# Kernel optimization log

Hardware: AMD Instinct MI355X
Metric: run time of the kernel (lower is better)

## Reference

```python
import jax, jax.numpy as jnp
import numpy as np

NEG_SLOPE = 0.2  # PyG GATConv default leaky_relu slope
N_NODES, IN_DIM, HID, HEADS, OUT = 50000, 128, 64, 4, 128
N_EDGES = 800000


def gat_conv(x, src, dst, num_nodes, W, a_src, a_dst, bias, concat):
    """One PyG-style GATConv (add_self_loops already applied to src/dst)."""
    H, C = a_src.shape
    xp = (x @ W).reshape(num_nodes, H, C)            # (N,H,C)
    s = jnp.einsum('nhc,hc->nh', xp, a_src)          # per-node src score
    d = jnp.einsum('nhc,hc->nh', xp, a_dst)          # per-node dst score
    e = s[src] + d[dst]                              # (E,H)
    e = jnp.where(e > 0, e, NEG_SLOPE * e)           # leaky_relu
    # segment softmax over edges grouped by destination node
    m = jax.ops.segment_max(e, dst, num_segments=num_nodes)
    p = jnp.exp(e - m[dst])
    z = jax.ops.segment_sum(p, dst, num_segments=num_nodes)
    alpha = p / (z[dst] + 1e-16)                     # (E,H)
    # scatter-aggregate messages
    out = jax.ops.segment_sum(xp[src] * alpha[:, :, None], dst, num_segments=num_nodes)
    out = out.reshape(num_nodes, H * C) if concat else out.mean(axis=1)
    return out + bias


def setup_inputs() -> dict:
    key = jax.random.key(0)
    ks = jax.random.split(key, 16)
    HC = HEADS * HID
    inp = {
        'x': jax.random.normal(ks[0], (N_NODES, IN_DIM), dtype=jnp.float32),
        'edge_index': jax.random.randint(ks[1], (2, N_EDGES), 0, N_NODES, dtype=jnp.int32),
        'W0': jax.random.normal(ks[2], (IN_DIM, HC), dtype=jnp.float32) * 0.08,
        'a_src0': jax.random.normal(ks[3], (HEADS, HID), dtype=jnp.float32) * 0.1,
        'a_dst0': jax.random.normal(ks[4], (HEADS, HID), dtype=jnp.float32) * 0.1,
        'b0': jnp.zeros((HC,), dtype=jnp.float32),
        'W1': jax.random.normal(ks[5], (HC, HC), dtype=jnp.float32) * 0.06,
        'a_src1': jax.random.normal(ks[6], (HEADS, HID), dtype=jnp.float32) * 0.1,
        'a_dst1': jax.random.normal(ks[7], (HEADS, HID), dtype=jnp.float32) * 0.1,
        'b1': jnp.zeros((HC,), dtype=jnp.float32),
        'W2': jax.random.normal(ks[8], (HC, OUT), dtype=jnp.float32) * 0.06,
        'a_src2': jax.random.normal(ks[9], (1, OUT), dtype=jnp.float32) * 0.1,
        'a_dst2': jax.random.normal(ks[10], (1, OUT), dtype=jnp.float32) * 0.1,
        'b2': jnp.zeros((OUT,), dtype=jnp.float32),
    }
    return inp


def reference(x, edge_index, W0, a_src0, a_dst0, b0, W1, a_src1, a_dst1, b1, W2, a_src2, a_dst2, b2):
    N = x.shape[0]
    loops = jnp.arange(N, dtype=edge_index.dtype)  # add_self_loops=True
    src = jnp.concatenate([edge_index[0], loops])
    dst = jnp.concatenate([edge_index[1], loops])
    h = gat_conv(x, src, dst, N, W0, a_src0, a_dst0, b0, True)
    h = jax.nn.elu(h)
    h = gat_conv(h, src, dst, N, W1, a_src1, a_dst1, b1, True)
    h = jax.nn.elu(h)
    h = gat_conv(h, src, dst, N, W2, a_src2, a_dst2, b2, False)
    return h
```

## Files before the change

### kernel.cpp

```cpp
#include <hip/hip_runtime.h>
#include <hip/hip_bf16.h>
#include <hip/hip_fp16.h>
#include <math.h>

#define N_NODES 50000
#define N_EDGES 800000
#define ET      (N_EDGES + N_NODES)
#define IN_DIM  128
#define HEADS   4
#define HID     64
#define HC      256
#define OUTD    128

typedef _Float16 half8 __attribute__((ext_vector_type(8)));
typedef float f32x4 __attribute__((ext_vector_type(4)));


__global__ void scan1_k(const int* __restrict__ counts, int* __restrict__ offs,
                        int* __restrict__ bsums) {
    __shared__ int sm[512];
    int tid = threadIdx.x;
    int i = blockIdx.x * 512 + tid;
    int v = (i < N_NODES) ? counts[i] : 0;
    sm[tid] = v;
    __syncthreads();
    #pragma unroll
    for (int o = 1; o < 512; o <<= 1) {
        int add = (tid >= o) ? sm[tid - o] : 0;
        __syncthreads();
        sm[tid] += add;
        __syncthreads();
    }
    if (i < N_NODES) offs[i] = sm[tid] - v;
    if (tid == 511) bsums[blockIdx.x] = sm[511];
}

__global__ void scan3_k(int* __restrict__ offs, const int* __restrict__ bsums) {
    __shared__ int base_sm;
    int tid = threadIdx.x;
    if (tid < 64) {
        int p = 0;
        for (int j = tid; j < (int)blockIdx.x; j += 64) p += bsums[j];
        #pragma unroll
        for (int o = 1; o < 64; o <<= 1) p += __shfl_xor(p, o, 64);
        if (tid == 0) base_sm = p;
    }
    __syncthreads();
    int i = blockIdx.x * 512 + tid;
    if (i < N_NODES) offs[i] += base_sm;
    if (i == 0) offs[N_NODES] = ET;
}

__global__ void fill_k(const int* __restrict__ ei, const int* __restrict__ offs,
                       int* __restrict__ counts, int* __restrict__ csr) {
    int i = blockIdx.x * blockDim.x + threadIdx.x;
    if (i >= ET) return;
    int sv, dv;
    if (i < N_EDGES) { sv = ei[i]; dv = ei[N_EDGES + i]; }
    else             { sv = dv = i - N_EDGES; }
    int pos = offs[dv] + atomicSub(&counts[dv], 1) - 1;
    csr[pos] = sv;
}


#define J_HIST  ET
#define J_CVT   (N_NODES * IN_DIM / 4)
#define J_W     131072
#define SETUP_TOTAL (J_HIST + J_CVT + J_W + 2 * N_NODES)

__global__ void setup_k(const int* __restrict__ ei, int* __restrict__ counts,
                        const float* __restrict__ x, __half* __restrict__ xh,
                        const float* __restrict__ W0, __half* __restrict__ Wt0,
                        const float* __restrict__ W1, __half* __restrict__ Wt1,
                        const float* __restrict__ W2, __half* __restrict__ Wt2,
                        float* __restrict__ S2, float* __restrict__ D2) {
    int g = blockIdx.x * 256 + threadIdx.x;
    if (g < J_HIST) {
        int dv = (g < N_EDGES) ? ei[N_EDGES + g] : (g - N_EDGES);
        atomicAdd(&counts[dv], 1);
        return;
    }
    g -= J_HIST;
    if (g < J_CVT) {
        float4 v = *(const float4*)(x + (size_t)g * 4);
        union { __half2 h2[2]; float2 f2; } u;
        u.h2[0] = __floats2half2_rn(v.x, v.y);
        u.h2[1] = __floats2half2_rn(v.z, v.w);
        *(float2*)(xh + (size_t)g * 4) = u.f2;
        return;
    }
    g -= J_CVT;
    if (g < J_W) {
        if (g < 32768) {
            int n = g / IN_DIM, k = g - n * IN_DIM;
            Wt0[g] = __float2half(W0[(size_t)k * HC + n]);
        } else if (g < 98304) {
            int i = g - 32768;
            int n = i / HC, k = i - n * HC;
            Wt1[i] = __float2half(W1[(size_t)k * HC + n]);
        } else {
            int i = g - 98304;
            int n = i / HC, k = i - n * HC;
            Wt2[i] = __float2half(W2[(size_t)k * OUTD + n]);
        }
        return;
    }
    g -= J_W;
    if (g < N_NODES) { S2[g] = 0.f; return; }
    g -= N_NODES;
    if (g < N_NODES) D2[g] = 0.f;
}


__device__ __forceinline__ void async_copy16(void* lds_base, const void* gaddr) {
    __builtin_amdgcn_global_load_lds(
        (const __attribute__((address_space(1))) unsigned int*)gaddr,
        (__attribute__((address_space(3))) unsigned int*)lds_base,
        16, 0, 0);
}

#define CPAD 132

template<int H, int CD, bool ATOMIC>
__global__ __launch_bounds__(256) void gemm_mfma_k(const __half* __restrict__ A,
                                                   const __half* __restrict__ Wt,
                                                   __half* __restrict__ C,
                                                   const float* __restrict__ asrc,
                                                   const float* __restrict__ adst,
                                                   float* __restrict__ S,
                                                   float* __restrict__ D,
                                                   int M, int K, int N) {
    __shared__ __attribute__((aligned(16))) __half smem[128 * CPAD];
    __half* Ah = smem;
    __half* Bh = smem + 128 * 64;
    const int t = threadIdx.x;
    const int w = t >> 6;
    const int lane = t & 63;
    const int wm = w >> 1, wn = w & 1;
    const int cc = lane & 15;
    const int quad = lane >> 4;
    const int row0 = blockIdx.x * 128;
    const int col0 = blockIdx.y * 128;

    f32x4 acc[4][4];
    #pragma unroll
    for (int i = 0; i < 4; ++i)
        #pragma unroll
        for (int j = 0; j < 4; ++j) acc[i][j] = (f32x4){0.f, 0.f, 0.f, 0.f};

    const int srow = lane >> 3;
    const int skq  = (lane & 7) * 8;

    for (int k0 = 0; k0 < K; k0 += 64) {
        __syncthreads();
        #pragma unroll
        for (int hh = 0; hh < 4; ++hh) {
            int ra = row0 + w * 32 + hh * 8 + srow;
            if (ra > M - 1) ra = M - 1;
            async_copy16(&Ah[(w * 32 + hh * 8) * 64],
                         A + (size_t)ra * K + k0 + skq);
            int rb = col0 + w * 32 + hh * 8 + srow;
            async_copy16(&Bh[(w * 32 + hh * 8) * 64],
                         Wt + (size_t)rb * K + k0 + skq);
        }
        __syncthreads();
        #pragma unroll
        for (int c = 0; c < 2; ++c) {
            half8 a[4], b[4];
            #pragma unroll
            for (int i = 0; i < 4; ++i)
                a[i] = *(const half8*)&Ah[(wm * 64 + i * 16 + cc) * 64 + c * 32 + quad * 8];
            #pragma unroll
            for (int j = 0; j < 4; ++j)
                b[j] = *(const half8*)&Bh[(wn * 64 + j * 16 + cc) * 64 + c * 32 + quad * 8];
            #pragma unroll
            for (int i = 0; i < 4; ++i)
                #pragma unroll
                for (int j = 0; j < 4; ++j)
                    acc[i][j] = __builtin_amdgcn_mfma_f32_16x16x32_f16(b[j], a[i], acc[i][j], 0, 0, 0);
        }
    }

    const int hh_ = ATOMIC ? 0 : (blockIdx.y * 2 + wn);
    float4 asj[4], adj[4];
    #pragma unroll
    for (int j = 0; j < 4; ++j) {
        int cb = (ATOMIC ? wn * 64 : 0) + j * 16 + quad * 4;
        asj[j] = *(const float4*)&asrc[hh_ * CD + cb];
        adj[j] = *(const float4*)&adst[hh_ * CD + cb];
    }
    #pragma unroll
    for (int i = 0; i < 4; ++i) {
        float sv = 0.f, dv = 0.f;
        #pragma unroll
        for (int j = 0; j < 4; ++j) {
            sv = fmaf(acc[i][j][0], asj[j].x, sv); dv = fmaf(acc[i][j][0], adj[j].x, dv);
            sv = fmaf(acc[i][j][1], asj[j].y, sv); dv = fmaf(acc[i][j][1], adj[j].y, dv);
            sv = fmaf(acc[i][j][2], asj[j].z, sv); dv = fmaf(acc[i][j][2], adj[j].z, dv);
            sv = fmaf(acc[i][j][3], asj[j].w, sv); dv = fmaf(acc[i][j][3], adj[j].w, dv);
        }
        sv += __shfl_xor(sv, 16, 64); dv += __shfl_xor(dv, 16, 64);
        sv += __shfl_xor(sv, 32, 64); dv += __shfl_xor(dv, 32, 64);
        int r = row0 + wm * 64 + i * 16 + cc;
        if (quad == 0 && r < M) {
            if constexpr (ATOMIC) {
                atomicAdd(&S[r], sv);
                atomicAdd(&D[r], dv);
            } else {
                S[(size_t)r * H + hh_] = sv;
                D[(size_t)r * H + hh_] = dv;
            }
        }
    }

    __syncthreads();
    #pragma unroll
    for (int i = 0; i < 4; ++i) {
        int tr = wm * 64 + i * 16 + cc;
        #pragma unroll
        for (int j = 0; j < 4; ++j) {
            int tc = wn * 64 + j * 16 + quad * 4;
            union { __half2 h2[2]; uint2 u2; } pk;
            pk.h2[0] = __floats2half2_rn(acc[i][j][0], acc[i][j][1]);
            pk.h2[1] = __floats2half2_rn(acc[i][j][2], acc[i][j][3]);
            *(uint2*)&smem[tr * CPAD + tc] = pk.u2;
        }
    }
    __syncthreads();
    #pragma unroll
    for (int rr = 0; rr < 8; ++rr) {
        int r = rr * 16 + (t >> 4);
        int ccol = (t & 15) * 8;
        uint4 v = *(const uint4*)&smem[r * CPAD + ccol];
        int gr = row0 + r;
        if (gr < M)
            *(uint4*)&C[(size_t)gr * N + col0 + ccol] = v;
    }
}


template<int H, int C, bool ELU_OUT, typename OT>
__global__ __launch_bounds__(256) void aggr_k(const __half* __restrict__ xp,
                                              const float* __restrict__ s,
                                              const float* __restrict__ d,
                                              const int* __restrict__ offs,
                                              const int* __restrict__ csr,
                                              const float* __restrict__ bias,
                                              OT* __restrict__ out) {
    constexpr int HCl = H * C;
    constexpr int EPL = HCl / 64;
    constexpr int U = 8;
    int wid = blockIdx.x * 4 + (threadIdx.x >> 6);
    int lane = threadIdx.x & 63;
    if (wid >= N_NODES) return;
    int h = (lane * EPL) / C;
    float dh = d[(size_t)wid * H + h];
    float z = 0.f;
    float acc[EPL];
    #pragma unroll
    for (int k = 0; k < EPL; ++k) acc[k] = 0.f;

    auto loadrow = [&](int src, float* v) {
        const __half* xr = xp + (size_t)src * HCl + lane * EPL;
        if constexpr (EPL == 4) {
            union { float2 f2; __half2 h2[2]; } u;
            u.f2 = *(const float2*)xr;
            float2 a = __half22float2(u.h2[0]);
            float2 b = __half22float2(u.h2[1]);
            v[0] = a.x; v[1] = a.y; v[2] = b.x; v[3] = b.y;
        } else {
            union { float f; __half2 h2; } u;
            u.f = *(const float*)xr;
            float2 a = __half22float2(u.h2);
            v[0] = a.x; v[1] = a.y;
        }
    };

    int e0 = offs[wid], e1 = offs[wid + 1];
    int j = e0;
    for (; j + U <= e1; j += U) {
        int srcs[U];
        #pragma unroll
        for (int u = 0; u < U; ++u) srcs[u] = csr[j + u];
        float ev[U];
        #pragma unroll
        for (int u = 0; u < U; ++u) ev[u] = s[(size_t)srcs[u] * H + h];
        float v[U][EPL];
        #pragma unroll
        for (int u = 0; u < U; ++u) loadrow(srcs[u], v[u]);
        #pragma unroll
        for (int u = 0; u < U; ++u) {
            float e = ev[u] + dh;
            e = (e > 0.f) ? e : 0.2f * e;
            float p = __expf(e);
            z += p;
            #pragma unroll
            for (int k = 0; k < EPL; ++k) acc[k] += p * v[u][k];
        }
    }
    for (; j < e1; ++j) {
        int sv = csr[j];
        float e = s[(size_t)sv * H + h] + dh;
        e = (e > 0.f) ? e : 0.2f * e;
        float p = __expf(e);
        float v[EPL];
        loadrow(sv, v);
        z += p;
        #pragma unroll
        for (int k = 0; k < EPL; ++k) acc[k] += p * v[k];
    }

    float inv = 1.f / (z + 1e-16f);
    float o[EPL];
    #pragma unroll
    for (int k = 0; k < EPL; ++k) {
        o[k] = acc[k] * inv + bias[lane * EPL + k];
        if constexpr (ELU_OUT) o[k] = (o[k] > 0.f) ? o[k] : (__expf(o[k]) - 1.f);
    }
    if constexpr (sizeof(OT) == 2 && EPL == 4) {
        union { __half2 h2[2]; float2 f2; } u;
        u.h2[0] = __floats2half2_rn(o[0], o[1]);
        u.h2[1] = __floats2half2_rn(o[2], o[3]);
        *(float2*)((__half*)out + (size_t)wid * HCl + lane * EPL) = u.f2;
    } else {
        #pragma unroll
        for (int k = 0; k < EPL; ++k)
            out[(size_t)wid * HCl + lane * EPL + k] = (OT)o[k];
    }
}


extern "C" void kernel_launch(void* const* d_in, const int* in_sizes, int n_in,
                              void* d_out, int out_size, void* d_ws, size_t ws_size,
                              hipStream_t stream) {
    const float* x      = (const float*)d_in[0];
    const int*   ei     = (const int*)  d_in[1];
    const float* W0     = (const float*)d_in[2];
    const float* as0    = (const float*)d_in[3];
    const float* ad0    = (const float*)d_in[4];
    const float* b0     = (const float*)d_in[5];
    const float* W1     = (const float*)d_in[6];
    const float* as1    = (const float*)d_in[7];
    const float* ad1    = (const float*)d_in[8];
    const float* b1     = (const float*)d_in[9];
    const float* W2     = (const float*)d_in[10];
    const float* as2    = (const float*)d_in[11];
    const float* ad2    = (const float*)d_in[12];
    const float* b2     = (const float*)d_in[13];
    float* out = (float*)d_out;

    char* p = (char*)d_ws;
    auto take = [&](size_t bytes) {
        char* r = p;
        p += (bytes + 255) & ~(size_t)255;
        return r;
    };
    __half* XPh   = (__half*)take((size_t)N_NODES * HC * 2);
    __half* Hbuf  = (__half*)take((size_t)N_NODES * HC * 2);
    __half* xh    = (__half*)take((size_t)N_NODES * IN_DIM * 2);
    __half* Wt0   = (__half*)take((size_t)IN_DIM * HC * 2);
    __half* Wt1   = (__half*)take((size_t)HC * HC * 2);
    __half* Wt2   = (__half*)take((size_t)HC * OUTD * 2);
    float*  S     = (float*) take((size_t)N_NODES * HEADS * 4);
    float*  D     = (float*) take((size_t)N_NODES * HEADS * 4);
    float*  S2    = (float*) take((size_t)N_NODES * 4);
    float*  D2    = (float*) take((size_t)N_NODES * 4);
    int*    counts= (int*)   take((size_t)N_NODES * 4);
    int*    offs  = (int*)   take((size_t)(N_NODES + 1) * 4);
    int*    bsums = (int*)   take(512 * 4);
    int*    csr   = (int*)   take((size_t)ET * 4);

    const int NB_SCAN = (N_NODES + 511) / 512;
    const int ET_BLOCKS = (ET + 255) / 256;
    const int NODE_BLOCKS = (N_NODES + 3) / 4;
    const int MB = (N_NODES + 127) / 128;
    dim3 g0(MB, HC / 128);
    dim3 g2(MB, OUTD / 128);

    hipMemsetAsync(counts, 0, (size_t)N_NODES * 4, stream);
    setup_k<<<(SETUP_TOTAL + 255) / 256, 256, 0, stream>>>(
        ei, counts, x, xh, W0, Wt0, W1, Wt1, W2, Wt2, S2, D2);

    scan1_k<<<NB_SCAN, 512, 0, stream>>>(counts, offs, bsums);
    scan3_k<<<NB_SCAN, 512, 0, stream>>>(offs, bsums);
    fill_k<<<ET_BLOCKS, 256, 0, stream>>>(ei, offs, counts, csr);

    gemm_mfma_k<HEADS, HID, false><<<g0, 256, 0, stream>>>(xh, Wt0, XPh, as0, ad0, S, D, N_NODES, IN_DIM, HC);
    aggr_k<HEADS, HID, true, __half><<<NODE_BLOCKS, 256, 0, stream>>>(XPh, S, D, offs, csr, b0, Hbuf);

    gemm_mfma_k<HEADS, HID, false><<<g0, 256, 0, stream>>>(Hbuf, Wt1, XPh, as1, ad1, S, D, N_NODES, HC, HC);
    aggr_k<HEADS, HID, true, __half><<<NODE_BLOCKS, 256, 0, stream>>>(XPh, S, D, offs, csr, b1, Hbuf);

    gemm_mfma_k<1, OUTD, true><<<g2, 256, 0, stream>>>(Hbuf, Wt2, XPh, as2, ad2, S2, D2, N_NODES, HC, OUTD);
    aggr_k<1, OUTD, false, float><<<NODE_BLOCKS, 256, 0, stream>>>(XPh, S2, D2, offs, csr, b2, out);
}
```

Baseline: 413.4 us.

## Split wavefront into two half-waves processing alternate edges with wider loads

The aggregation kernel now splits each 64-lane wavefront into two 32-lane halves. Each half handles alternate edges of the destination node, and each lane loads 8 or 4 halves per row (16- or 8-byte vector loads) instead of 4 or 2. Partial sums are combined with a cross-half shuffle, and the remainder loop is replaced by predicated masking that sets the score of out-of-range edges to a large negative value. The aim is more memory parallelism per wave and wider gathers, at the cost of padded wasted work on short edge lists and an extra reduction.

```diff
diff --git a/kernel.cpp b/kernel.cpp
--- a/kernel.cpp
+++ b/kernel.cpp
@@ -248,84 +248,96 @@
                                               const float* __restrict__ bias,
                                               OT* __restrict__ out) {
     constexpr int HCl = H * C;
-    constexpr int EPL = HCl / 64;
+    constexpr int FPL = HCl / 32;
     constexpr int U = 8;
-    int wid = blockIdx.x * 4 + (threadIdx.x >> 6);
-    int lane = threadIdx.x & 63;
+    const int tid = threadIdx.x;
+    const int lane = tid & 63;
+    const int l = lane & 31;
+    const int par = lane >> 5;
+    int wid = blockIdx.x * 4 + (tid >> 6);
     if (wid >= N_NODES) return;
-    int h = (lane * EPL) / C;
-    float dh = d[(size_t)wid * H + h];
+    const int h = (l * FPL) / C;
+    const int loff = l * FPL;
+
+    float dh = d[wid * H + h];
     float z = 0.f;
-    float acc[EPL];
-    #pragma unroll
-    for (int k = 0; k < EPL; ++k) acc[k] = 0.f;
-
-    auto loadrow = [&](int src, float* v) {
-        const __half* xr = xp + (size_t)src * HCl + lane * EPL;
-        if constexpr (EPL == 4) {
-            union { float2 f2; __half2 h2[2]; } u;
-            u.f2 = *(const float2*)xr;
-            float2 a = __half22float2(u.h2[0]);
-            float2 b = __half22float2(u.h2[1]);
-            v[0] = a.x; v[1] = a.y; v[2] = b.x; v[3] = b.y;
-        } else {
-            union { float f; __half2 h2; } u;
-            u.f = *(const float*)xr;
-            float2 a = __half22float2(u.h2);
-            v[0] = a.x; v[1] = a.y;
-        }
-    };
-
-    int e0 = offs[wid], e1 = offs[wid + 1];
-    int j = e0;
-    for (; j + U <= e1; j += U) {
-        int srcs[U];
-        #pragma unroll
-        for (int u = 0; u < U; ++u) srcs[u] = csr[j + u];
-        float ev[U];
-        #pragma unroll
-        for (int u = 0; u < U; ++u) ev[u] = s[(size_t)srcs[u] * H + h];
-        float v[U][EPL];
-        #pragma unroll
-        for (int u = 0; u < U; ++u) loadrow(srcs[u], v[u]);
-        #pragma unroll
-        for (int u = 0; u < U; ++u) {
-            float e = ev[u] + dh;
-            e = (e > 0.f) ? e : 0.2f * e;
-            float p = __expf(e);
-            z += p;
-            #pragma unroll
-            for (int k = 0; k < EPL; ++k) acc[k] += p * v[u][k];
-        }
-    }
-    for (; j < e1; ++j) {
-        int sv = csr[j];
-        float e = s[(size_t)sv * H + h] + dh;
-        e = (e > 0.f) ? e : 0.2f * e;
-        float p = __expf(e);
-        float v[EPL];
-        loadrow(sv, v);
-        z += p;
-        #pragma unroll
-        for (int k = 0; k < EPL; ++k) acc[k] += p * v[k];
-    }
+    float acc[FPL];
+    #pragma unroll
+    for (int k = 0; k < FPL; ++k) acc[k] = 0.f;
+
+    const int e0 = offs[wid];
+    const int e1 = offs[wid + 1];
+
+    for (int j = e0; j < e1; j += U) {
+        int ss[4];
+        #pragma unroll
+        for (int k2 = 0; k2 < 4; ++k2) {
+            int idx = j + 2 * k2 + par;
+            ss[k2] = csr[idx < e1 ? idx : e1 - 1];
+        }
+        float ev[4];
+        #pragma unroll
+        for (int k2 = 0; k2 < 4; ++k2)
+            ev[k2] = s[ss[k2] * H + h];
+        uint4 r4[4];
+        uint2 r2[4];
+        #pragma unroll
+        for (int k2 = 0; k2 < 4; ++k2) {
+            const __half* rowp = xp + (size_t)ss[k2] * HCl + loff;
+            if constexpr (FPL == 8) r4[k2] = *(const uint4*)rowp;
+            else                    r2[k2] = *(const uint2*)rowp;
+        }
+        #pragma unroll
+        for (int k2 = 0; k2 < 4; ++k2) {
+            float e = (j + 2 * k2 + par < e1) ? (ev[k2] + dh) : -1e30f;
+            e = fmaxf(e, 0.2f * e);
+            float pw = __expf(e);
+            z += pw;
+            if constexpr (FPL == 8) {
+                union { uint4 u; __half2 h2[4]; } rr; rr.u = r4[k2];
+                #pragma unroll
+                for (int q = 0; q < 4; ++q) {
+                    acc[2*q]   = fmaf(pw, __half2float(__low2half(rr.h2[q])),  acc[2*q]);
+                    acc[2*q+1] = fmaf(pw, __half2float(__high2half(rr.h2[q])), acc[2*q+1]);
+                }
+            } else {
+                union { uint2 u; __half2 h2[2]; } rr; rr.u = r2[k2];
+                #pragma unroll
+                for (int q = 0; q < 2; ++q) {
+                    acc[2*q]   = fmaf(pw, __half2float(__low2half(rr.h2[q])),  acc[2*q]);
+                    acc[2*q+1] = fmaf(pw, __half2float(__high2half(rr.h2[q])), acc[2*q+1]);
+                }
+            }
+        }
+    }
+
+    z += __shfl_xor(z, 32, 64);
+    #pragma unroll
+    for (int k = 0; k < FPL; ++k) acc[k] += __shfl_xor(acc[k], 32, 64);
+
+    if (lane >= 32) return;
 
     float inv = 1.f / (z + 1e-16f);
-    float o[EPL];
-    #pragma unroll
-    for (int k = 0; k < EPL; ++k) {
-        o[k] = acc[k] * inv + bias[lane * EPL + k];
+    float o[FPL];
+    #pragma unroll
+    for (int k = 0; k < FPL; ++k) {
+        o[k] = acc[k] * inv + bias[loff + k];
         if constexpr (ELU_OUT) o[k] = (o[k] > 0.f) ? o[k] : (__expf(o[k]) - 1.f);
     }
-    if constexpr (sizeof(OT) == 2 && EPL == 4) {
-        union { __half2 h2[2]; float2 f2; } u;
+    if constexpr (sizeof(OT) == 2 && FPL == 8) {
+        union { __half2 h2[4]; uint4 u4; } u;
         u.h2[0] = __floats2half2_rn(o[0], o[1]);
         u.h2[1] = __floats2half2_rn(o[2], o[3]);
-        *(float2*)((__half*)out + (size_t)wid * HCl + lane * EPL) = u.f2;
+        u.h2[2] = __floats2half2_rn(o[4], o[5]);
+        u.h2[3] = __floats2half2_rn(o[6], o[7]);
+        *(uint4*)((__half*)out + (size_t)wid * HCl + loff) = u.u4;
+    } else if constexpr (sizeof(OT) == 4 && FPL == 4) {
+        float4 v; v.x = o[0]; v.y = o[1]; v.z = o[2]; v.w = o[3];
+        *(float4*)((float*)out + (size_t)wid * HCl + loff) = v;
     } else {
         #pragma unroll
-        for (int k = 0; k < EPL; ++k)
-            out[(size_t)wid * HCl + lane * EPL + k] = (OT)o[k];
+        for (int k = 0; k < FPL; ++k)
+            out[(size_t)wid * HCl + loff + k] = (OT)o[k];
     }
 }
 
```

Measured after the change: 388.8 us. -6.0%, faster.
